# Performance work log

Hardware: AMD Instinct MI355X
Metric: run time of the kernel (lower is better)

## Reference

```python
import jax, jax.numpy as jnp
import numpy as np

B, M = 2, 4096
N1, N2, N3 = 16384, 8192, 4096
OFFSET = (0.0, -40.0, -3.0)
LR_VS = (0.4, 0.4, 1.0)
HR1_VS = (0.05, 0.05, 0.1)
HR2_VS = (0.1, 0.1, 0.2)
HR3_VS = (0.2, 0.2, 0.4)
RADIUS = 1.0
NS1, NS2, NS3 = 128, 32, 16
BN_EPS = 1e-3


def _rand_idx(key, n, dims):
    kz, ky, kx = jax.random.split(key, 3)
    z = jax.random.randint(kz, (B, n, 1), 0, dims[0], dtype=jnp.int32)
    y = jax.random.randint(ky, (B, n, 1), 0, dims[1], dtype=jnp.int32)
    x = jax.random.randint(kx, (B, n, 1), 0, dims[2], dtype=jnp.int32)
    return jnp.concatenate([z, y, x], axis=-1)


def setup_inputs() -> dict:
    key = jax.random.key(0)
    ks = jax.random.split(key, 16)
    s = 0.1
    inp = {}
    # voxel indices are (z, y, x) per the original coors layout
    inp["lr_idx"] = _rand_idx(ks[0], M, (5, 200, 176))
    inp["hr1_idx"] = _rand_idx(ks[1], N1, (40, 1600, 1408))
    inp["hr2_idx"] = _rand_idx(ks[2], N2, (20, 800, 704))
    inp["hr3_idx"] = _rand_idx(ks[3], N3, (10, 400, 352))
    inp["lr_feat"] = jax.random.normal(ks[4], (B, M, 64), jnp.float32)
    inp["hr1_feat"] = jax.random.normal(ks[5], (B, N1, 16), jnp.float32)
    inp["hr2_feat"] = jax.random.normal(ks[6], (B, N2, 32), jnp.float32)
    inp["hr3_feat"] = jax.random.normal(ks[7], (B, N3, 64), jnp.float32)
    # Grouper shared-MLP weights (single layer each; +3 channels for use_xyz)
    inp["w14"] = jax.random.normal(ks[8], (19, 32), jnp.float32) * s
    inp["b14"] = jnp.zeros((32,), jnp.float32)
    inp["w24"] = jax.random.normal(ks[9], (35, 32), jnp.float32) * s
    inp["b24"] = jnp.zeros((32,), jnp.float32)
    inp["w34"] = jax.random.normal(ks[10], (67, 32), jnp.float32) * s
    inp["b34"] = jnp.zeros((32,), jnp.float32)
    # conv4_out: 1x1x1 sparse conv == dense matmul per voxel, then BN + ReLU
    inp["w_out"] = jax.random.normal(ks[11], (160, 64), jnp.float32) * s
    inp["bn_gamma"] = jnp.ones((64,), jnp.float32)
    inp["bn_beta"] = jnp.zeros((64,), jnp.float32)
    inp["bn_mean"] = jnp.zeros((64,), jnp.float32)
    inp["bn_var"] = jnp.ones((64,), jnp.float32)
    return inp


def idx_to_xyz(idx, vs):
    # indices are (z,y,x); original does indices[:, [3,2,1]] * voxel_size + offset + 0.5*voxel_size
    vs = jnp.asarray(vs, jnp.float32)
    off = jnp.asarray(OFFSET, jnp.float32)
    return idx[..., ::-1].astype(jnp.float32) * vs + off + 0.5 * vs


def ball_query(lr_xyz, hr_xyz, nsample):
    # first-nsample-within-radius semantics of pointnet2 ball_query
    d2 = jnp.sum((lr_xyz[:, None, :] - hr_xyz[None, :, :]) ** 2, axis=-1)  # [M, N]
    n = hr_xyz.shape[0]
    cand = jnp.where(d2 < RADIUS * RADIUS, jnp.arange(n, dtype=jnp.int32), n)
    neg, _ = jax.lax.top_k(-cand, nsample)  # smallest nsample candidate indices
    idx = -neg
    idx = jnp.where(idx == n, idx[:, :1], idx)  # pad with first valid neighbor
    return jnp.where(idx == n, 0, idx)          # no neighbor at all -> index 0


def group_pool(lr_xyz, hr_xyz, hr_feat, nsample, w, b):
    idx = ball_query(lr_xyz, hr_xyz, nsample)          # [M, ns]
    g_xyz = hr_xyz[idx] - lr_xyz[:, None, :]           # [M, ns, 3] relative coords
    g = jnp.concatenate([g_xyz, hr_feat[idx]], axis=-1)  # [M, ns, 3+C]
    h = jax.nn.relu(jnp.einsum('msc,co->mso', g, w) + b)
    return h.max(axis=1)                                # [M, Cout] max-pool over neighbors


def reference(lr_idx, hr1_idx, hr2_idx, hr3_idx, lr_feat, hr1_feat, hr2_feat, hr3_feat,
              w14, b14, w24, b24, w34, b34, w_out, bn_gamma, bn_beta, bn_mean, bn_var):
    lr_xyz = idx_to_xyz(lr_idx, LR_VS)                  # [B, M, 3]
    f14 = jax.vmap(lambda l, h, f: group_pool(l, h, f, NS1, w14, b14))(lr_xyz, idx_to_xyz(hr1_idx, HR1_VS), hr1_feat)
    f24 = jax.vmap(lambda l, h, f: group_pool(l, h, f, NS2, w24, b24))(lr_xyz, idx_to_xyz(hr2_idx, HR2_VS), hr2_feat)
    f34 = jax.vmap(lambda l, h, f: group_pool(l, h, f, NS3, w34, b34))(lr_xyz, idx_to_xyz(hr3_idx, HR3_VS), hr3_feat)
    cat = jnp.concatenate([lr_feat, f14, f24, f34], axis=-1)  # [B, M, 160] (in-place feature growth)
    y = jnp.einsum('bmc,co->bmo', cat, w_out)
    y = (y - bn_mean) * jax.lax.rsqrt(bn_var + BN_EPS) * bn_gamma + bn_beta
    return jax.nn.relu(y)
```

## Files before the change

kernel.cpp:

```cpp
#include <hip/hip_runtime.h>

#define BM   8192
#define NN1  16384
#define NN2  8192
#define NN3  4096
#define NB   80
#define TSZ  768
#define QCAP 512

#define OFF_LRS   0
#define OFF_S1    32768
#define OFF_S2    163840
#define OFF_S3    229376
#define OFF_F1    262144
#define OFF_F2    1310720
#define OFF_F3    1835008
#define OFF_START 2097152
#define OFF_WP    2098176
#define OFF_SHIFT 2108416
#define WS_FLOATS 2108480

__global__ __launch_bounds__(256) void kprep(
    const int* __restrict__ lr_idx, const int* __restrict__ h1i,
    const int* __restrict__ h2i, const int* __restrict__ h3i,
    const float* __restrict__ f1, const float* __restrict__ f2, const float* __restrict__ f3,
    const float* __restrict__ w14, const float* __restrict__ b14,
    const float* __restrict__ w24, const float* __restrict__ b24,
    const float* __restrict__ w34, const float* __restrict__ b34,
    const float* __restrict__ wout, const float* __restrict__ gam,
    const float* __restrict__ bet, const float* __restrict__ mean,
    const float* __restrict__ var, float* __restrict__ ws)
{
    __shared__ int hist[NB];
    __shared__ int stt[NB+1];
    __shared__ int cur[NB];
    int bx = blockIdx.x, tid = threadIdx.x;

    if (bx < 8) {
        int t = bx;
        int N, ibase, dst4; const int* ip; float vsx, vsz; bool isLR = (t >= 6);
        if (t < 2)      { N=NN1; ip=h1i; ibase=(t&1)*NN1; vsx=0.05f; vsz=0.1f; dst4=OFF_S1/4+(t&1)*NN1; }
        else if (t < 4) { N=NN2; ip=h2i; ibase=(t&1)*NN2; vsx=0.1f;  vsz=0.2f; dst4=OFF_S2/4+(t&1)*NN2; }
        else if (t < 6) { N=NN3; ip=h3i; ibase=(t&1)*NN3; vsx=0.2f;  vsz=0.4f; dst4=OFF_S3/4+(t&1)*NN3; }
        else            { N=4096; ip=lr_idx; ibase=(t&1)*4096; vsx=0.4f; vsz=1.0f; dst4=OFF_LRS/4+(t&1)*4096; }

        if (tid < NB) hist[tid] = 0;
        __syncthreads();
        for (int e = tid; e < N; e += 256) {
            int iy = ip[(ibase+e)*3 + 1];
            float y = __fadd_rn(__fadd_rn(__fmul_rn((float)iy, vsx), -40.0f), __fmul_rn(0.5f, vsx));
            int k = min(NB-1, max(0, (int)floorf(y + 40.0f)));
            atomicAdd(&hist[k], 1);
        }
        __syncthreads();
        if (tid < 64) {
            int v = hist[tid];
            #pragma unroll
            for (int s = 1; s < 64; s <<= 1) { int u = __shfl_up(v, s); if (tid >= s) v += u; }
            int base64 = __shfl(v, 63);
            int v2 = (tid < 16) ? hist[64 + tid] : 0;
            #pragma unroll
            for (int s = 1; s < 16; s <<= 1) { int u = __shfl_up(v2, s); if (tid >= s) v2 += u; }
            if (tid == 0) stt[0] = 0;
            stt[1 + tid] = v;
            if (tid < 16) stt[65 + tid] = base64 + v2;
        }
        __syncthreads();
        if (tid < NB) cur[tid] = stt[tid];
        if (tid < NB+1) reinterpret_cast<int*>(ws)[OFF_START + t*81 + tid] = stt[tid];
        __syncthreads();
        for (int e = tid; e < N; e += 256) {
            int r3 = (ibase+e)*3;
            int iz = ip[r3], iy = ip[r3+1], ix = ip[r3+2];
            float4 v;
            v.x = __fadd_rn(__fadd_rn(__fmul_rn((float)ix, vsx),   0.0f), __fmul_rn(0.5f, vsx));
            v.y = __fadd_rn(__fadd_rn(__fmul_rn((float)iy, vsx), -40.0f), __fmul_rn(0.5f, vsx));
            v.z = __fadd_rn(__fadd_rn(__fmul_rn((float)iz, vsz),  -3.0f), __fmul_rn(0.5f, vsz));
            v.w = __int_as_float(isLR ? (ibase + e) : e);
            int k = min(NB-1, max(0, (int)floorf(v.y + 40.0f)));
            int pos = atomicAdd(&cur[k], 1);
            reinterpret_cast<float4*>(ws)[dst4 + pos] = v;
        }
        return;
    }

    int e = (bx - 8) * 256 + tid;

    if (e < 262144) {
        int o2 = e & 7, jj = e >> 3;
        const float4* fv = reinterpret_cast<const float4*>(f1) + jj*4;
        const float4* w4 = reinterpret_cast<const float4*>(w14);
        float4 acc = reinterpret_cast<const float4*>(b14)[o2];
        float fr[16];
        #pragma unroll
        for (int c4 = 0; c4 < 4; ++c4) {
            float4 f = fv[c4];
            fr[c4*4] = f.x; fr[c4*4+1] = f.y; fr[c4*4+2] = f.z; fr[c4*4+3] = f.w;
        }
        #pragma unroll
        for (int c = 0; c < 16; ++c) {
            float4 w = w4[(3+c)*8 + o2];
            acc.x = fmaf(fr[c], w.x, acc.x); acc.y = fmaf(fr[c], w.y, acc.y);
            acc.z = fmaf(fr[c], w.z, acc.z); acc.w = fmaf(fr[c], w.w, acc.w);
        }
        reinterpret_cast<float4*>(ws + OFF_F1)[jj*8 + o2] = acc;
        return;
    }
    e -= 262144;
    if (e < 131072) {
        int o2 = e & 7, jj = e >> 3;
        const float4* fv = reinterpret_cast<const float4*>(f2) + jj*8;
        const float4* w4 = reinterpret_cast<const float4*>(w24);
        float4 acc = reinterpret_cast<const float4*>(b24)[o2];
        #pragma unroll
        for (int cc = 0; cc < 32; cc += 16) {
            float fr[16];
            #pragma unroll
            for (int c4 = 0; c4 < 4; ++c4) {
                float4 f = fv[cc/4 + c4];
                fr[c4*4] = f.x; fr[c4*4+1] = f.y; fr[c4*4+2] = f.z; fr[c4*4+3] = f.w;
            }
            #pragma unroll
            for (int c = 0; c < 16; ++c) {
                float4 w = w4[(3+cc+c)*8 + o2];
                acc.x = fmaf(fr[c], w.x, acc.x); acc.y = fmaf(fr[c], w.y, acc.y);
                acc.z = fmaf(fr[c], w.z, acc.z); acc.w = fmaf(fr[c], w.w, acc.w);
            }
        }
        reinterpret_cast<float4*>(ws + OFF_F2)[jj*8 + o2] = acc;
        return;
    }
    e -= 131072;
    if (e < 65536) {
        int o2 = e & 7, jj = e >> 3;
        const float4* fv = reinterpret_cast<const float4*>(f3) + jj*16;
        const float4* w4 = reinterpret_cast<const float4*>(w34);
        float4 acc = reinterpret_cast<const float4*>(b34)[o2];
        #pragma unroll
        for (int cc = 0; cc < 64; cc += 16) {
            float fr[16];
            #pragma unroll
            for (int c4 = 0; c4 < 4; ++c4) {
                float4 f = fv[cc/4 + c4];
                fr[c4*4] = f.x; fr[c4*4+1] = f.y; fr[c4*4+2] = f.z; fr[c4*4+3] = f.w;
            }
            #pragma unroll
            for (int c = 0; c < 16; ++c) {
                float4 w = w4[(3+cc+c)*8 + o2];
                acc.x = fmaf(fr[c], w.x, acc.x); acc.y = fmaf(fr[c], w.y, acc.y);
                acc.z = fmaf(fr[c], w.z, acc.z); acc.w = fmaf(fr[c], w.w, acc.w);
            }
        }
        reinterpret_cast<float4*>(ws + OFF_F3)[jj*8 + o2] = acc;
        return;
    }
    e -= 65536;

    if (e < 10240) {
        int o = e & 63;
        float sc = gam[o] * (1.0f / sqrtf(var[o] + 1e-3f));
        ws[OFF_WP + e] = wout[e] * sc;
    } else if (e < 10304) {
        int o = e - 10240;
        float sc = gam[o] * (1.0f / sqrtf(var[o] + 1e-3f));
        ws[OFF_SHIFT + o] = bet[o] - mean[o] * sc;
    }
}

__global__ __launch_bounds__(512) void kscan(
    float* __restrict__ ws, const float* __restrict__ lr_feat,
    const int* __restrict__ h1i, const int* __restrict__ h2i, const int* __restrict__ h3i,
    const float* __restrict__ w14, const float* __restrict__ w24, const float* __restrict__ w34,
    float* __restrict__ out)
{
    __shared__ float4 Sst[TSZ];
    __shared__ float  catS[32][160];
    __shared__ int    accS[32*33];
    __shared__ float  lrS[32*4];
    __shared__ float  wAll[288];
    __shared__ int    cntS[32];
    __shared__ int    porigS[32];
    __shared__ int    queue[QCAP];
    __shared__ int    qn;

    int pg = blockIdx.x;
    int b  = pg >> 7;
    int tid = threadIdx.x, lane = tid & 63, half = lane >> 5, p = lane & 31, wv = tid >> 6;

    if (tid < 96)        wAll[tid]       = w14[tid];
    else if (tid < 192)  wAll[tid]       = w24[tid-96];
    else if (tid < 288)  wAll[tid-192+192] = w34[tid-192];
    for (int e = tid; e < 32*33; e += 512) accS[e] = 0;
    if (tid < 32) {
        float4 l = reinterpret_cast<const float4*>(ws + OFF_LRS)[pg*32 + tid];
        reinterpret_cast<float4*>(lrS)[tid] = l;
        porigS[tid] = __float_as_int(l.w);
        cntS[tid] = 0;
    }
    if (tid == 0) qn = 0;

    float4 lr = reinterpret_cast<const float4*>(ws + OFF_LRS)[pg*32 + p];
    float ymin = lr.y, ymax = lr.y;
    #pragma unroll
    for (int m = 1; m < 32; m <<= 1) {
        ymin = fminf(ymin, __shfl_xor(ymin, m));
        ymax = fmaxf(ymax, __shfl_xor(ymax, m));
    }
    int klo = max(0, (int)floorf(ymin - 1.001f + 40.0f));
    int khi = min(NB-1, (int)floorf(ymax + 1.001f + 40.0f));

    __syncthreads();

    for (int e = tid; e < 2048; e += 512) {
        int i = e >> 6, c = e & 63;
        catS[i][c] = lr_feat[porigS[i]*64 + c];
    }

    #pragma unroll 1
    for (int s = 0; s < 3; ++s) {
        const int* hidx; int soff, Foff, N, wb; float vsx, vsz;
        if (s == 0)      { hidx=h1i; soff=OFF_S1; Foff=OFF_F1; N=NN1; vsx=0.05f; vsz=0.1f; wb=0; }
        else if (s == 1) { hidx=h2i; soff=OFF_S2; Foff=OFF_F2; N=NN2; vsx=0.1f;  vsz=0.2f; wb=96; }
        else             { hidx=h3i; soff=OFF_S3; Foff=OFF_F3; N=NN3; vsx=0.2f;  vsz=0.4f; wb=192; }

        const int* st = reinterpret_cast<const int*>(ws) + OFF_START + (s*2+b)*81;
        int j0 = st[klo], j1 = st[khi+1];
        const float4* S  = reinterpret_cast<const float4*>(ws + soff) + b*N;
        const float* Fb = ws + Foff + (size_t)b*N*32;

        for (int t0 = j0; t0 < j1; t0 += TSZ) {
            int tlen = min(TSZ, j1 - t0);
            __syncthreads();
            for (int e = tid; e < tlen; e += 512) Sst[e] = S[t0 + e];
            __syncthreads();

            int a   = (tlen * wv) >> 3;
            int bnd = (tlen * (wv+1)) >> 3;
            for (int j = a + half; j < bnd; j += 2) {
                float4 q = Sst[j];
                float dx = q.x - lr.x, dy = q.y - lr.y, dz = q.z - lr.z;
                float d2 = __fadd_rn(__fadd_rn(__fmul_rn(dx,dx), __fmul_rn(dy,dy)), __fmul_rn(dz,dz));
                if (d2 < 1.0f) {
                    cntS[p] = 1;
                    int pos = atomicAdd(&qn, 1);
                    if (pos < QCAP) queue[pos] = (j << 5) | p;
                }
            }
            __syncthreads();

            int nh = min(qn, QCAP);
            for (int e = tid; e < nh*32; e += 512) {
                int ent = queue[e >> 5], o = e & 31;
                int jl = ent >> 5, pp = ent & 31;
                float4 q = Sst[jl];
                float dx = q.x - lrS[pp*4], dy = q.y - lrS[pp*4+1], dz = q.z - lrS[pp*4+2];
                int jo = __float_as_int(q.w);
                float h = Fb[(size_t)jo*32 + o] + dx*wAll[wb+o] + dy*wAll[wb+32+o] + dz*wAll[wb+64+o];
                atomicMax(&accS[pp*33 + o], __float_as_int(h));
            }
            __syncthreads();
            if (tid == 0) qn = 0;
        }

        int i0 = b * N * 3;
        int hz = hidx[i0], hy = hidx[i0+1], hx = hidx[i0+2];
        float q0x = __fadd_rn(__fadd_rn(__fmul_rn((float)hx, vsx),   0.0f), __fmul_rn(0.5f, vsx));
        float q0y = __fadd_rn(__fadd_rn(__fmul_rn((float)hy, vsx), -40.0f), __fmul_rn(0.5f, vsx));
        float q0z = __fadd_rn(__fadd_rn(__fmul_rn((float)hz, vsz),  -3.0f), __fmul_rn(0.5f, vsz));

        for (int e = tid; e < 1024; e += 512) {
            int i = e >> 5, o = e & 31;
            float v;
            if (cntS[i]) v = __int_as_float(accS[i*33 + o]);
            else {
                float dx = q0x - lrS[i*4], dy = q0y - lrS[i*4+1], dz = q0z - lrS[i*4+2];
                v = fmaxf(Fb[o] + dx*wAll[wb+o] + dy*wAll[wb+32+o] + dz*wAll[wb+64+o], 0.f);
            }
            catS[i][64 + s*32 + o] = v;
        }
        __syncthreads();
        for (int e = tid; e < 32*33; e += 512) accS[e] = 0;
        if (tid < 32) cntS[tid] = 0;
    }
    __syncthreads();

    float sh = ws[OFF_SHIFT + lane];
    float acc[4] = {sh, sh, sh, sh};
    const float* wp = ws + OFF_WP;
    #pragma unroll 2
    for (int c = 0; c < 160; c += 4) {
        float w0 = wp[(c+0)*64 + lane];
        float w1 = wp[(c+1)*64 + lane];
        float w2 = wp[(c+2)*64 + lane];
        float w3 = wp[(c+3)*64 + lane];
        #pragma unroll
        for (int pt = 0; pt < 4; ++pt) {
            float4 cv = *reinterpret_cast<const float4*>(&catS[wv*4 + pt][c]);
            acc[pt] = fmaf(cv.x, w0, acc[pt]);
            acc[pt] = fmaf(cv.y, w1, acc[pt]);
            acc[pt] = fmaf(cv.z, w2, acc[pt]);
            acc[pt] = fmaf(cv.w, w3, acc[pt]);
        }
    }
    #pragma unroll
    for (int pt = 0; pt < 4; ++pt)
        out[porigS[wv*4 + pt]*64 + lane] = fmaxf(acc[pt], 0.f);
}

extern "C" void kernel_launch(void* const* d_in, const int* in_sizes, int n_in,
                              void* d_out, int out_size, void* d_ws, size_t ws_size,
                              hipStream_t stream) {
    const int*   lr_idx = (const int*)d_in[0];
    const int*   h1i    = (const int*)d_in[1];
    const int*   h2i    = (const int*)d_in[2];
    const int*   h3i    = (const int*)d_in[3];
    const float* lrf    = (const float*)d_in[4];
    const float* f1     = (const float*)d_in[5];
    const float* f2     = (const float*)d_in[6];
    const float* f3     = (const float*)d_in[7];
    const float* w14    = (const float*)d_in[8];
    const float* b14    = (const float*)d_in[9];
    const float* w24    = (const float*)d_in[10];
    const float* b24    = (const float*)d_in[11];
    const float* w34    = (const float*)d_in[12];
    const float* b34    = (const float*)d_in[13];
    const float* wout   = (const float*)d_in[14];
    const float* gam    = (const float*)d_in[15];
    const float* bet    = (const float*)d_in[16];
    const float* mean   = (const float*)d_in[17];
    const float* var    = (const float*)d_in[18];
    float* ws  = (float*)d_ws;
    float* out = (float*)d_out;

    if (ws_size < (size_t)WS_FLOATS * sizeof(float)) return;

    kprep<<<1841, 256, 0, stream>>>(lr_idx, h1i, h2i, h3i, f1, f2, f3,
                                    w14, b14, w24, b24, w34, b34,
                                    wout, gam, bet, mean, var, ws);
    kscan<<<256, 512, 0, stream>>>(ws, lrf, h1i, h2i, h3i, w14, w24, w34, out);
}
```

Measured before the change: 164.2 us.

## Parallelize y-bin counting sort across 32 blocks with a separate scatter kernel

Replaces the 8-block per-table histogram and scatter in kprep with a 32-block parallel histogram over all tables. A new ksort kernel reduces the partial histograms, computes per-block prefix offsets, and scatters the converted points in parallel. The old version serialized the large hr1 tables on single blocks and likely sat on the critical path. In exchange it adds a third kernel launch and a global round-trip for the partial histograms. Within-bin order now depends on atomics across blocks.

```diff
diff --git a/kernel.cpp b/kernel.cpp
--- a/kernel.cpp
+++ b/kernel.cpp
@@ -5,6 +5,8 @@
 #define NN2  8192
 #define NN3  4096
 #define NB   80
+#define NBLK 32
+#define CHUNK 2048
 #define TSZ  768
 #define QCAP 512
 
@@ -15,10 +17,12 @@
 #define OFF_F1    262144
 #define OFF_F2    1310720
 #define OFF_F3    1835008
-#define OFF_START 2097152
-#define OFF_WP    2098176
-#define OFF_SHIFT 2108416
-#define WS_FLOATS 2108480
+#define OFF_PART  2097152
+#define OFF_START 2117632
+#define OFF_WP    2118656
+#define OFF_SHIFT 2128896
+#define WS_FLOATS 2128960
+
 
 __global__ __launch_bounds__(256) void kprep(
     const int* __restrict__ lr_idx, const int* __restrict__ h1i,
@@ -31,60 +35,35 @@
     const float* __restrict__ bet, const float* __restrict__ mean,
     const float* __restrict__ var, float* __restrict__ ws)
 {
-    __shared__ int hist[NB];
-    __shared__ int stt[NB+1];
-    __shared__ int cur[NB];
+    __shared__ int hist[640];
     int bx = blockIdx.x, tid = threadIdx.x;
 
-    if (bx < 8) {
-        int t = bx;
-        int N, ibase, dst4; const int* ip; float vsx, vsz; bool isLR = (t >= 6);
-        if (t < 2)      { N=NN1; ip=h1i; ibase=(t&1)*NN1; vsx=0.05f; vsz=0.1f; dst4=OFF_S1/4+(t&1)*NN1; }
-        else if (t < 4) { N=NN2; ip=h2i; ibase=(t&1)*NN2; vsx=0.1f;  vsz=0.2f; dst4=OFF_S2/4+(t&1)*NN2; }
-        else if (t < 6) { N=NN3; ip=h3i; ibase=(t&1)*NN3; vsx=0.2f;  vsz=0.4f; dst4=OFF_S3/4+(t&1)*NN3; }
-        else            { N=4096; ip=lr_idx; ibase=(t&1)*4096; vsx=0.4f; vsz=1.0f; dst4=OFF_LRS/4+(t&1)*4096; }
-
-        if (tid < NB) hist[tid] = 0;
+    if (bx < NBLK) {
+        for (int e = tid; e < 640; e += 256) hist[e] = 0;
         __syncthreads();
-        for (int e = tid; e < N; e += 256) {
-            int iy = ip[(ibase+e)*3 + 1];
+        int base_it = bx * CHUNK;
+        for (int t = tid; t < CHUNK; t += 256) {
+            int e = base_it + t;
+            int T, iy; float vsx;
+            if (e < 8192)            { T = 6 + (e>>12); iy = lr_idx[e*3+1]; vsx = 0.4f; }
+            else { int r = e - 8192;
+              if (r < 32768)         { int b = r>>14; T = b;   iy = h1i[r*3+1]; vsx = 0.05f; }
+              else { r -= 32768;
+                if (r < 16384)       { int b = r>>13; T = 2+b; iy = h2i[r*3+1]; vsx = 0.1f; }
+                else { r -= 16384; int b = r>>12; T = 4+b; iy = h3i[r*3+1]; vsx = 0.2f; }
+              }
+            }
             float y = __fadd_rn(__fadd_rn(__fmul_rn((float)iy, vsx), -40.0f), __fmul_rn(0.5f, vsx));
             int k = min(NB-1, max(0, (int)floorf(y + 40.0f)));
-            atomicAdd(&hist[k], 1);
+            atomicAdd(&hist[T*80 + k], 1);
         }
         __syncthreads();
-        if (tid < 64) {
-            int v = hist[tid];
-            #pragma unroll
-            for (int s = 1; s < 64; s <<= 1) { int u = __shfl_up(v, s); if (tid >= s) v += u; }
-            int base64 = __shfl(v, 63);
-            int v2 = (tid < 16) ? hist[64 + tid] : 0;
-            #pragma unroll
-            for (int s = 1; s < 16; s <<= 1) { int u = __shfl_up(v2, s); if (tid >= s) v2 += u; }
-            if (tid == 0) stt[0] = 0;
-            stt[1 + tid] = v;
-            if (tid < 16) stt[65 + tid] = base64 + v2;
-        }
-        __syncthreads();
-        if (tid < NB) cur[tid] = stt[tid];
-        if (tid < NB+1) reinterpret_cast<int*>(ws)[OFF_START + t*81 + tid] = stt[tid];
-        __syncthreads();
-        for (int e = tid; e < N; e += 256) {
-            int r3 = (ibase+e)*3;
-            int iz = ip[r3], iy = ip[r3+1], ix = ip[r3+2];
-            float4 v;
-            v.x = __fadd_rn(__fadd_rn(__fmul_rn((float)ix, vsx),   0.0f), __fmul_rn(0.5f, vsx));
-            v.y = __fadd_rn(__fadd_rn(__fmul_rn((float)iy, vsx), -40.0f), __fmul_rn(0.5f, vsx));
-            v.z = __fadd_rn(__fadd_rn(__fmul_rn((float)iz, vsz),  -3.0f), __fmul_rn(0.5f, vsz));
-            v.w = __int_as_float(isLR ? (ibase + e) : e);
-            int k = min(NB-1, max(0, (int)floorf(v.y + 40.0f)));
-            int pos = atomicAdd(&cur[k], 1);
-            reinterpret_cast<float4*>(ws)[dst4 + pos] = v;
-        }
+        for (int e = tid; e < 640; e += 256)
+            reinterpret_cast<int*>(ws)[OFF_PART + bx*640 + e] = hist[e];
         return;
     }
 
-    int e = (bx - 8) * 256 + tid;
+    int e = (bx - NBLK) * 256 + tid;
 
     if (e < 262144) {
         int o2 = e & 7, jj = e >> 3;
@@ -167,7 +146,73 @@
     }
 }
 
-__global__ __launch_bounds__(512) void kscan(
+__global__ __launch_bounds__(1024) void ksort(
+    const int* __restrict__ lr_idx, const int* __restrict__ h1i,
+    const int* __restrict__ h2i, const int* __restrict__ h3i,
+    float* __restrict__ ws)
+{
+    __shared__ int totS[640];
+    __shared__ int stt[648];
+    __shared__ int cur[640];
+    int t = threadIdx.x, bx = blockIdx.x;
+    int* wsi = reinterpret_cast<int*>(ws);
+
+    int tot = 0, mypre = 0;
+    if (t < 640) {
+        #pragma unroll
+        for (int b = 0; b < NBLK; ++b) {
+            int p = wsi[OFF_PART + b*640 + t];
+            tot += p;
+            if (b < bx) mypre += p;
+        }
+        totS[t] = tot;
+    }
+    __syncthreads();
+    int wid = t >> 6, lane = t & 63;
+    if (wid < 8) {
+        int v = totS[wid*80 + lane];
+        #pragma unroll
+        for (int s = 1; s < 64; s <<= 1) { int u = __shfl_up(v, s); if (lane >= s) v += u; }
+        int base64 = __shfl(v, 63);
+        int v2 = (lane < 16) ? totS[wid*80 + 64 + lane] : 0;
+        #pragma unroll
+        for (int s = 1; s < 16; s <<= 1) { int u = __shfl_up(v2, s); if (lane >= s) v2 += u; }
+        if (lane == 0) stt[wid*81] = 0;
+        stt[wid*81 + 1 + lane] = v;
+        if (lane < 16) stt[wid*81 + 65 + lane] = base64 + v2;
+    }
+    __syncthreads();
+    if (bx == 0 && t < 648) wsi[OFF_START + t] = stt[t];
+    if (t < 640) cur[t] = stt[(t/80)*81 + (t%80)] + mypre;
+    __syncthreads();
+
+    int base_it = bx * CHUNK;
+    for (int tt = t; tt < CHUNK; tt += 1024) {
+        int e = base_it + tt;
+        int T, w, dst4, r3; const int* ip; float vsx, vsz;
+        if (e < 8192) {
+            int b = e >> 12; T = 6+b; ip = lr_idx; r3 = e*3; vsx = 0.4f; vsz = 1.0f;
+            w = e; dst4 = OFF_LRS/4 + b*4096;
+        } else { int r = e - 8192;
+          if (r < 32768) { int b = r>>14; T = b;   ip = h1i; r3 = r*3; vsx = 0.05f; vsz = 0.1f; w = r - b*NN1; dst4 = OFF_S1/4 + b*NN1; }
+          else { r -= 32768;
+            if (r < 16384) { int b = r>>13; T = 2+b; ip = h2i; r3 = r*3; vsx = 0.1f; vsz = 0.2f; w = r - b*NN2; dst4 = OFF_S2/4 + b*NN2; }
+            else { r -= 16384; int b = r>>12; T = 4+b; ip = h3i; r3 = r*3; vsx = 0.2f; vsz = 0.4f; w = r - b*NN3; dst4 = OFF_S3/4 + b*NN3; }
+          }
+        }
+        int iz = ip[r3], iy = ip[r3+1], ix = ip[r3+2];
+        float4 v;
+        v.x = __fadd_rn(__fadd_rn(__fmul_rn((float)ix, vsx),   0.0f), __fmul_rn(0.5f, vsx));
+        v.y = __fadd_rn(__fadd_rn(__fmul_rn((float)iy, vsx), -40.0f), __fmul_rn(0.5f, vsx));
+        v.z = __fadd_rn(__fadd_rn(__fmul_rn((float)iz, vsz),  -3.0f), __fmul_rn(0.5f, vsz));
+        v.w = __int_as_float(w);
+        int k = min(NB-1, max(0, (int)floorf(v.y + 40.0f)));
+        int pos = atomicAdd(&cur[T*80 + k], 1);
+        reinterpret_cast<float4*>(ws)[dst4 + pos] = v;
+    }
+}
+
+__global__ __launch_bounds__(512) void kmain(
     float* __restrict__ ws, const float* __restrict__ lr_feat,
     const int* __restrict__ h1i, const int* __restrict__ h2i, const int* __restrict__ h3i,
     const float* __restrict__ w14, const float* __restrict__ w24, const float* __restrict__ w34,
@@ -187,9 +232,9 @@
     int b  = pg >> 7;
     int tid = threadIdx.x, lane = tid & 63, half = lane >> 5, p = lane & 31, wv = tid >> 6;
 
-    if (tid < 96)        wAll[tid]       = w14[tid];
-    else if (tid < 192)  wAll[tid]       = w24[tid-96];
-    else if (tid < 288)  wAll[tid-192+192] = w34[tid-192];
+    if (tid < 96)        wAll[tid] = w14[tid];
+    else if (tid < 192)  wAll[tid] = w24[tid-96];
+    else if (tid < 288)  wAll[tid] = w34[tid-192];
     for (int e = tid; e < 32*33; e += 512) accS[e] = 0;
     if (tid < 32) {
         float4 l = reinterpret_cast<const float4*>(ws + OFF_LRS)[pg*32 + tid];
@@ -334,8 +379,9 @@
 
     if (ws_size < (size_t)WS_FLOATS * sizeof(float)) return;
 
-    kprep<<<1841, 256, 0, stream>>>(lr_idx, h1i, h2i, h3i, f1, f2, f3,
+    kprep<<<1865, 256, 0, stream>>>(lr_idx, h1i, h2i, h3i, f1, f2, f3,
                                     w14, b14, w24, b24, w34, b34,
                                     wout, gam, bet, mean, var, ws);
-    kscan<<<256, 512, 0, stream>>>(ws, lrf, h1i, h2i, h3i, w14, w24, w34, out);
+    ksort<<<NBLK, 1024, 0, stream>>>(lr_idx, h1i, h2i, h3i, ws);
+    kmain<<<256, 512, 0, stream>>>(ws, lrf, h1i, h2i, h3i, w14, w24, w34, out);
 }
```

Result: faster. 140.8 us, median of 2 (-14.3%).
